# Optimization experiments

Measured on AMD Instinct MI355X. Metric: run time of the kernel, lower is better.

Reference implementation:

```python
import jax, jax.numpy as jnp
import numpy as np

B, S, D = 2, 2048, 1024   # batch, seq, d_model
E, K, H = 8, 4, 1024      # experts, top-k, expert hidden
SH = 2 * H                # shared-expert hidden (n_shared_experts=2)


def setup_inputs() -> dict:
    key = jax.random.key(0)
    ks = jax.random.split(key, 24)
    f = lambda k, shape: jax.random.normal(k, shape, dtype=jnp.float32) * 0.02
    return {
        "x": jax.random.normal(ks[0], (B, S, D), dtype=jnp.float32),
        # Linear(in_features, out_features), stored as [in, out]
        "lin0_w": f(ks[1], (D, D)), "lin0_b": f(ks[2], (D,)),
        "swi1_w1": f(ks[3], (D, D)), "swi1_b1": f(ks[4], (D,)),
        "swi1_w2": f(ks[5], (D, D)), "swi1_b2": f(ks[6], (D,)),
        # MoE router (no bias) + routed experts (SwiGLU FFN, no bias)
        "gate_w": f(ks[7], (E, D)),
        "exp_w1": f(ks[8], (E, D, H)),
        "exp_w3": f(ks[9], (E, D, H)),
        "exp_w2": f(ks[10], (E, H, D)),
        # shared experts fused into one wider SwiGLU MLP (2 shared experts)
        "sh_w1": f(ks[11], (D, SH)),
        "sh_w3": f(ks[12], (D, SH)),
        "sh_w2": f(ks[13], (SH, D)),
        # second Linear + SwiGLU block (num_ff=2)
        "lin1_w": f(ks[14], (D, D)), "lin1_b": f(ks[15], (D,)),
        "swi2_w1": f(ks[16], (D, D)), "swi2_b1": f(ks[17], (D,)),
        "swi2_w2": f(ks[18], (D, D)), "swi2_b2": f(ks[19], (D,)),
    }


def _silu(x):
    return x * jax.nn.sigmoid(x)


def _swiglu(x, w1, b1, w2, b2):
    return _silu(x @ w1 + b1) * (x @ w2 + b2)


def _moe(x, gate_w, exp_w1, exp_w3, exp_w2, sh_w1, sh_w3, sh_w2):
    b, s, d = x.shape
    t = b * s
    xt = x.reshape(t, d)
    # router: softmax scores, greedy top-k, normalized weights (scaling factor = 1)
    scores = jax.nn.softmax(xt @ gate_w.T, axis=-1)          # [T, E]
    topv, topi = jax.lax.top_k(scores, K)                    # [T, K]
    topv = topv / jnp.sum(topv, axis=-1, keepdims=True)
    combine = jnp.zeros((t, E), xt.dtype).at[jnp.arange(t)[:, None], topi].set(topv)  # [T, E]
    # routed experts: SwiGLU FFN per expert, dense-masked combine (same math as dispatch)
    g = _silu(jnp.einsum('td,edh->eth', xt, exp_w1))
    u = jnp.einsum('td,edh->eth', xt, exp_w3)
    yexp = jnp.einsum('eth,ehd->etd', g * u, exp_w2)         # [E, T, D]
    routed = jnp.einsum('te,etd->td', combine, yexp)         # [T, D]
    # shared experts (always on)
    shared = (_silu(xt @ sh_w1) * (xt @ sh_w3)) @ sh_w2      # [T, D]
    return (routed + shared).reshape(b, s, d)


def reference(x, lin0_w, lin0_b, swi1_w1, swi1_b1, swi1_w2, swi1_b2,
              gate_w, exp_w1, exp_w3, exp_w2, sh_w1, sh_w3, sh_w2,
              lin1_w, lin1_b, swi2_w1, swi2_b1, swi2_w2, swi2_b2):
    h = x @ lin0_w + lin0_b
    h = _swiglu(h, swi1_w1, swi1_b1, swi1_w2, swi1_b2)
    h = _moe(h, gate_w, exp_w1, exp_w3, exp_w2, sh_w1, sh_w3, sh_w2)
    h = h @ lin1_w + lin1_b
    h = _swiglu(h, swi2_w1, swi2_b1, swi2_w2, swi2_b2)
    return h
```

## Files before the change

kernel.cpp:

```cpp
#include <hip/hip_runtime.h>
#include <cstdint>
#include <cstddef>

#define T_TOKENS 4096
#define D_MODEL  1024
#define N_EXP    8
#define TOP_K    4
#define H_EXP    1024
#define SH_HID   2048
#define TK       (T_TOKENS*TOP_K)

typedef __bf16 bf16x8 __attribute__((ext_vector_type(8)));
typedef __bf16 bf16x4 __attribute__((ext_vector_type(4)));
typedef float  f32x4  __attribute__((ext_vector_type(4)));

__device__ __forceinline__ float silu_f(float x) {
    return x / (1.0f + expf(-x));
}

template<int NT, bool SEG, bool GATHER, bool GLU>
__global__ __launch_bounds__(256)
void gemm_sp(const float* __restrict__ A, int lda,
             const float* __restrict__ W1, const float* __restrict__ W3,
             int64_t w_estride, int ldw,
             const float* __restrict__ bias1, const float* __restrict__ bias2,
             float* __restrict__ C, __bf16* __restrict__ Cb1, int ldc,
             int M, int Kd,
             const int* __restrict__ seg_off,
             const int* __restrict__ gather)
{
    constexpr int BM = 128, BN = 128, BK = 32;
    __shared__ __bf16 Asl[NT][BM * BK];
    __shared__ __bf16 Bsl[NT][BN * BK];

    int m0, m1, e = 0;
    if (SEG) {
        e = blockIdx.z;
        int s0 = seg_off[e], s1 = seg_off[e + 1];
        m0 = s0 + blockIdx.y * BM;
        if (m0 >= s1) return;
        m1 = (m0 + BM < s1) ? (m0 + BM) : s1;
    } else {
        m0 = blockIdx.y * BM;
        m1 = (m0 + BM < M) ? (m0 + BM) : M;
    }
    const int n0 = blockIdx.x * BN;

    const int tid  = threadIdx.x;
    const int lane = tid & 63;
    const int w    = tid >> 6;
    const int wm   = w >> 1, wn = w & 1;
    const int fr   = lane & 15, fq = lane >> 4;

    const float* aP[4]; int aR[4], aQ[4];
#pragma unroll
    for (int i = 0; i < 4; ++i) {
        int Li = tid + 256 * i;
        int r = Li >> 3, q = Li & 7;
        aR[i] = r; aQ[i] = q;
        int grow = m0 + r;
        if (grow > m1 - 1) grow = m1 - 1;
        if (GATHER) grow = gather[grow];
        aP[i] = A + (int64_t)grow * lda + q * 4;
    }

    const int bn  = tid & 127;
    const int bkh = tid >> 7;
    const float* Wsrc; int wcol;
    if (GLU) {
        int cl = n0 + bn;
        int B  = cl >> 4;
        Wsrc = (B & 1) ? W3 : W1;
        wcol = ((B >> 1) << 4) | (cl & 15);
    } else {
        Wsrc = W1; wcol = n0 + bn;
    }
    const float* Wb = Wsrc + (int64_t)e * w_estride + (int64_t)(bkh * 16) * ldw + wcol;

    f32x4 zero4 = {0.f, 0.f, 0.f, 0.f};
    f32x4 acc[4][4];
#pragma unroll
    for (int i = 0; i < 4; ++i)
#pragma unroll
        for (int j = 0; j < 4; ++j) acc[i][j] = zero4;

    float4 av[4];
    float  wv[16];

#define GLOADS(K0)                                                         \
    do {                                                                   \
        _Pragma("unroll")                                                  \
        for (int i = 0; i < 4; ++i)                                        \
            av[i] = *reinterpret_cast<const float4*>(aP[i] + (K0));        \
        _Pragma("unroll")                                                  \
        for (int j = 0; j < 16; ++j)                                       \
            wv[j] = Wb[(int64_t)((K0) + j) * ldw];                         \
    } while (0)

    const int nk = Kd / BK;
    GLOADS(0);

    for (int ks = 0; ks < nk; ++ks) {
        bf16x4 pa[NT][4];
        bf16x4 pw[NT][4];
#pragma unroll
        for (int i = 0; i < 4; ++i) {
            float vv[4] = {av[i].x, av[i].y, av[i].z, av[i].w};
#pragma unroll
            for (int t = 0; t < 4; ++t) {
                float v = vv[t];
                __bf16 h = (__bf16)v;
                pa[0][i][t] = h;
                if (NT >= 2) {
                    float r = v - (float)h;
                    if (NT == 2) {
                        pa[1][i][t] = (__bf16)r;
                    } else {
                        __bf16 m = (__bf16)r;
                        pa[1][i][t] = m;
                        pa[2][i][t] = (__bf16)(r - (float)m);
                    }
                }
            }
        }
#pragma unroll
        for (int qd = 0; qd < 4; ++qd) {
#pragma unroll
            for (int t = 0; t < 4; ++t) {
                float v = wv[qd * 4 + t];
                __bf16 h = (__bf16)v;
                pw[0][qd][t] = h;
                if (NT >= 2) {
                    float r = v - (float)h;
                    if (NT == 2) {
                        pw[1][qd][t] = (__bf16)r;
                    } else {
                        __bf16 m = (__bf16)r;
                        pw[1][qd][t] = m;
                        pw[2][qd][t] = (__bf16)(r - (float)m);
                    }
                }
            }
        }

        __syncthreads();
#pragma unroll
        for (int i = 0; i < 4; ++i) {
            int r = aR[i], q = aQ[i];
            int c = (q >> 1) ^ ((r >> 1) & 3);
            int idx = r * BK + c * 8 + (q & 1) * 4;
#pragma unroll
            for (int p = 0; p < NT; ++p)
                *reinterpret_cast<bf16x4*>(&Asl[p][idx]) = pa[p][i];
        }
#pragma unroll
        for (int qd = 0; qd < 4; ++qd) {
            int q32 = bkh * 4 + qd;
            int c = (q32 >> 1) ^ ((bn >> 1) & 3);
            int idx = bn * BK + c * 8 + (q32 & 1) * 4;
#pragma unroll
            for (int p = 0; p < NT; ++p)
                *reinterpret_cast<bf16x4*>(&Bsl[p][idx]) = pw[p][qd];
        }

        if (ks + 1 < nk) GLOADS((ks + 1) * BK);
        __syncthreads();

        bf16x8 bfr[NT][4];
#pragma unroll
        for (int p = 0; p < NT; ++p)
#pragma unroll
            for (int j = 0; j < 4; ++j) {
                int rown = wn * 64 + j * 16 + fr;
                int c = fq ^ ((rown >> 1) & 3);
                bfr[p][j] = *reinterpret_cast<const bf16x8*>(&Bsl[p][rown * BK + c * 8]);
            }
#pragma unroll
        for (int im = 0; im < 4; ++im) {
            bf16x8 af[NT];
            int rowm = wm * 64 + im * 16 + fr;
            int c = fq ^ ((rowm >> 1) & 3);
#pragma unroll
            for (int p = 0; p < NT; ++p)
                af[p] = *reinterpret_cast<const bf16x8*>(&Asl[p][rowm * BK + c * 8]);
#pragma unroll
            for (int jn = 0; jn < 4; ++jn) {
                f32x4 a = acc[im][jn];
                a = __builtin_amdgcn_mfma_f32_16x16x32_bf16(af[0], bfr[0][jn], a, 0, 0, 0);
                if (NT >= 2) {
                    a = __builtin_amdgcn_mfma_f32_16x16x32_bf16(af[0], bfr[1][jn], a, 0, 0, 0);
                    a = __builtin_amdgcn_mfma_f32_16x16x32_bf16(af[1], bfr[0][jn], a, 0, 0, 0);
                }
                if (NT == 3) {
                    a = __builtin_amdgcn_mfma_f32_16x16x32_bf16(af[1], bfr[1][jn], a, 0, 0, 0);
                    a = __builtin_amdgcn_mfma_f32_16x16x32_bf16(af[0], bfr[2][jn], a, 0, 0, 0);
                    a = __builtin_amdgcn_mfma_f32_16x16x32_bf16(af[2], bfr[0][jn], a, 0, 0, 0);
                }
                acc[im][jn] = a;
            }
        }
    }
#undef GLOADS

    if (GLU) {
#pragma unroll
        for (int jn = 0; jn < 4; jn += 2) {
            int gcol = (n0 >> 1) + wn * 32 + (jn >> 1) * 16 + fr;
            float bv1 = bias1 ? bias1[gcol] : 0.f;
            float bv2 = bias2 ? bias2[gcol] : 0.f;
#pragma unroll
            for (int im = 0; im < 4; ++im) {
                f32x4 v1 = acc[im][jn];
                f32x4 v2 = acc[im][jn + 1];
#pragma unroll
                for (int r = 0; r < 4; ++r) {
                    int grow = m0 + wm * 64 + im * 16 + fq * 4 + r;
                    if (grow < m1) {
                        float val = silu_f(v1[r] + bv1) * (v2[r] + bv2);
                        int64_t o = (int64_t)grow * ldc + gcol;
                        C[o] = val;
                        if (Cb1) Cb1[o] = (__bf16)val;
                    }
                }
            }
        }
    } else {
#pragma unroll
        for (int jn = 0; jn < 4; ++jn) {
            int col = n0 + wn * 64 + jn * 16 + fr;
            float bv = bias1 ? bias1[col] : 0.f;
#pragma unroll
            for (int im = 0; im < 4; ++im) {
                f32x4 v = acc[im][jn];
#pragma unroll
                for (int r = 0; r < 4; ++r) {
                    int grow = m0 + wm * 64 + im * 16 + fq * 4 + r;
                    if (grow < m1)
                        C[(int64_t)grow * ldc + col] = v[r] + bv;
                }
            }
        }
    }
}

template<bool WBF, bool SEG, bool GATHER, bool GLU, bool EMITB>
__global__ __launch_bounds__(256)
void gemm_bb(const __bf16* __restrict__ A, int lda,
             const void* __restrict__ W1v, const void* __restrict__ W3v,
             int64_t w_estride, int ldw,
             float* __restrict__ C, __bf16* __restrict__ Cb, int ldc,
             int M, int Kd,
             const int* __restrict__ seg_off,
             const int* __restrict__ gather)
{
    constexpr int BM = 128, BN = 128, BK = 32;
    __shared__ __bf16 Asl[BM * BK];
    __shared__ __bf16 Bsl[BN * BK];

    int m0, m1, e = 0;
    if (SEG) {
        e = blockIdx.z;
        int s0 = seg_off[e], s1 = seg_off[e + 1];
        m0 = s0 + blockIdx.y * BM;
        if (m0 >= s1) return;
        m1 = (m0 + BM < s1) ? (m0 + BM) : s1;
    } else {
        m0 = blockIdx.y * BM;
        m1 = (m0 + BM < M) ? (m0 + BM) : M;
    }
    const int n0 = blockIdx.x * BN;

    const int tid  = threadIdx.x;
    const int lane = tid & 63;
    const int w    = tid >> 6;
    const int wm   = w >> 1, wn = w & 1;
    const int fr   = lane & 15, fq = lane >> 4;

    int aWr[2]; const __bf16* Ab[2];
#pragma unroll
    for (int i = 0; i < 2; ++i) {
        int L = tid + 256 * i;
        int r = L >> 2, ch = L & 3;
        aWr[i] = r * BK + (ch ^ ((r >> 1) & 3)) * 8;
        int grow = m0 + r;
        if (grow > m1 - 1) grow = m1 - 1;
        if (GATHER) grow = gather[grow];
        Ab[i] = A + (int64_t)grow * lda + ch * 8;
    }

    const int bn  = tid & 127;
    const int bkh = tid >> 7;
    int wcol; const void* Wsel;
    if (GLU) {
        int cl = n0 + bn;
        int B  = cl >> 4;
        Wsel = (B & 1) ? W3v : W1v;
        wcol = ((B >> 1) << 4) | (cl & 15);
    } else {
        Wsel = W1v; wcol = n0 + bn;
    }
    const __bf16* Wbb = nullptr; const float* Wbf = nullptr;
    if (WBF) Wbb = (const __bf16*)Wsel + (int64_t)e * w_estride + (int64_t)(bkh * 16) * ldw + wcol;
    else     Wbf = (const float*)Wsel + (int64_t)e * w_estride + (int64_t)(bkh * 16) * ldw + wcol;
    int wWr[2];
#pragma unroll
    for (int c = 0; c < 2; ++c)
        wWr[c] = bn * BK + ((bkh * 2 + c) ^ ((bn >> 1) & 3)) * 8;

    f32x4 zero4 = {0.f, 0.f, 0.f, 0.f};
    f32x4 acc[4][4];
#pragma unroll
    for (int i = 0; i < 4; ++i)
#pragma unroll
        for (int j = 0; j < 4; ++j) acc[i][j] = zero4;

    bf16x8 areg[2];
    bf16x8 wreg[2];

#define GLOADS(K0)                                                          \
    do {                                                                    \
        areg[0] = *reinterpret_cast<const bf16x8*>(Ab[0] + (K0));           \
        areg[1] = *reinterpret_cast<const bf16x8*>(Ab[1] + (K0));           \
        if (WBF) {                                                          \
            _Pragma("unroll")                                               \
            for (int j = 0; j < 16; ++j)                                    \
                wreg[j >> 3][j & 7] = Wbb[(int64_t)((K0) + j) * ldw];       \
        } else {                                                            \
            _Pragma("unroll")                                               \
            for (int j = 0; j < 16; ++j)                                    \
                wreg[j >> 3][j & 7] = (__bf16)Wbf[(int64_t)((K0) + j) * ldw]; \
        }                                                                   \
    } while (0)

    const int nk = Kd / BK;
    GLOADS(0);

    for (int ks = 0; ks < nk; ++ks) {
        __syncthreads();
        *reinterpret_cast<bf16x8*>(&Asl[aWr[0]]) = areg[0];
        *reinterpret_cast<bf16x8*>(&Asl[aWr[1]]) = areg[1];
        *reinterpret_cast<bf16x8*>(&Bsl[wWr[0]]) = wreg[0];
        *reinterpret_cast<bf16x8*>(&Bsl[wWr[1]]) = wreg[1];
        if (ks + 1 < nk) GLOADS((ks + 1) * BK);
        __syncthreads();

        bf16x8 bfr[4];
#pragma unroll
        for (int j = 0; j < 4; ++j) {
            int rown = wn * 64 + j * 16 + fr;
            int c = fq ^ ((rown >> 1) & 3);
            bfr[j] = *reinterpret_cast<const bf16x8*>(&Bsl[rown * BK + c * 8]);
        }
#pragma unroll
        for (int im = 0; im < 4; ++im) {
            int rowm = wm * 64 + im * 16 + fr;
            int c = fq ^ ((rowm >> 1) & 3);
            bf16x8 af = *reinterpret_cast<const bf16x8*>(&Asl[rowm * BK + c * 8]);
#pragma unroll
            for (int jn = 0; jn < 4; ++jn)
                acc[im][jn] = __builtin_amdgcn_mfma_f32_16x16x32_bf16(af, bfr[jn], acc[im][jn], 0, 0, 0);
        }
    }
#undef GLOADS

    if (GLU) {
#pragma unroll
        for (int jn = 0; jn < 4; jn += 2) {
            int gcol = (n0 >> 1) + wn * 32 + (jn >> 1) * 16 + fr;
#pragma unroll
            for (int im = 0; im < 4; ++im) {
                f32x4 v1 = acc[im][jn];
                f32x4 v2 = acc[im][jn + 1];
#pragma unroll
                for (int r = 0; r < 4; ++r) {
                    int grow = m0 + wm * 64 + im * 16 + fq * 4 + r;
                    if (grow < m1) {
                        float val = silu_f(v1[r]) * v2[r];
                        int64_t o = (int64_t)grow * ldc + gcol;
                        if (EMITB) Cb[o] = (__bf16)val;
                        else       C[o]  = val;
                    }
                }
            }
        }
    } else {
#pragma unroll
        for (int jn = 0; jn < 4; ++jn) {
            int col = n0 + wn * 64 + jn * 16 + fr;
#pragma unroll
            for (int im = 0; im < 4; ++im) {
                f32x4 v = acc[im][jn];
#pragma unroll
                for (int r = 0; r < 4; ++r) {
                    int grow = m0 + wm * 64 + im * 16 + fq * 4 + r;
                    if (grow < m1)
                        C[(int64_t)grow * ldc + col] = v[r];
                }
            }
        }
    }
}

__global__ void f2b(const float* __restrict__ s, __bf16* __restrict__ d, int64_t n4)
{
    int64_t i = (int64_t)blockIdx.x * blockDim.x + threadIdx.x;
    int64_t st = (int64_t)gridDim.x * blockDim.x;
    for (; i < n4; i += st) {
        float4 v = reinterpret_cast<const float4*>(s)[i];
        bf16x4 o;
        o[0] = (__bf16)v.x; o[1] = (__bf16)v.y;
        o[2] = (__bf16)v.z; o[3] = (__bf16)v.w;
        reinterpret_cast<bf16x4*>(d)[i] = o;
    }
}

__global__ __launch_bounds__(256)
void router_logits(const float* __restrict__ h1, const float* __restrict__ gw,
                   int* __restrict__ topi, float* __restrict__ topw,
                   unsigned char* __restrict__ emask)
{
    const int wave = threadIdx.x >> 6, lane = threadIdx.x & 63;
    const int t = blockIdx.x * 4 + wave;
    const float* x = h1 + (int64_t)t * D_MODEL;
    float part[N_EXP];
#pragma unroll
    for (int e = 0; e < N_EXP; ++e) part[e] = 0.f;
#pragma unroll 4
    for (int i = 0; i < D_MODEL / 64; ++i) {
        int d = lane + 64 * i;
        float xv = x[d];
#pragma unroll
        for (int e = 0; e < N_EXP; ++e)
            part[e] = fmaf(xv, gw[e * D_MODEL + d], part[e]);
    }
#pragma unroll
    for (int m = 32; m > 0; m >>= 1)
#pragma unroll
        for (int e = 0; e < N_EXP; ++e)
            part[e] += __shfl_xor(part[e], m, 64);

    if (lane == 0) {
        float p[N_EXP];
        float mx = -1e30f;
#pragma unroll
        for (int e = 0; e < N_EXP; ++e) mx = part[e] > mx ? part[e] : mx;
        float z = 0.f;
#pragma unroll
        for (int e = 0; e < N_EXP; ++e) { p[e] = expf(part[e] - mx); z += p[e]; }
#pragma unroll
        for (int e = 0; e < N_EXP; ++e) p[e] /= z;
        bool used[N_EXP];
#pragma unroll
        for (int e = 0; e < N_EXP; ++e) used[e] = false;
        int sel[TOP_K]; float sv[TOP_K]; float wsum = 0.f;
        unsigned m8 = 0;
        for (int k = 0; k < TOP_K; ++k) {
            int best = 0; float bvv = -1.f;
            for (int e = 0; e < N_EXP; ++e)
                if (!used[e] && p[e] > bvv) { bvv = p[e]; best = e; }
            used[best] = true; sel[k] = best; sv[k] = bvv; wsum += bvv;
            m8 |= 1u << best;
        }
        for (int k = 0; k < TOP_K; ++k) {
            int idx = t * TOP_K + k;
            topi[idx] = sel[k];
            topw[idx] = sv[k] / wsum;
        }
        emask[t] = (unsigned char)m8;
    }
}

__global__ __launch_bounds__(256)
void rank_local(const unsigned char* __restrict__ emask,
                const int* __restrict__ topi,
                int* __restrict__ pose, int* __restrict__ bh)
{
    const int b = blockIdx.x;
    const int t = b * 256 + threadIdx.x;
    const int wave = threadIdx.x >> 6, lane = threadIdx.x & 63;
    const unsigned m8 = emask[t];

    __shared__ int wcnt[4][N_EXP];
    __shared__ int wbase[4][N_EXP];
    int lrank[N_EXP];
#pragma unroll
    for (int e = 0; e < N_EXP; ++e) {
        unsigned long long bal = __ballot((m8 >> e) & 1u);
        lrank[e] = __popcll(bal & ((1ull << lane) - 1ull));
        if (lane == 0) wcnt[wave][e] = __popcll(bal);
    }
    __syncthreads();
    if (threadIdx.x < N_EXP) {
        int e = threadIdx.x; int a = 0;
        for (int wv = 0; wv < 4; ++wv) { wbase[wv][e] = a; a += wcnt[wv][e]; }
        bh[b * N_EXP + e] = a;
    }
    __syncthreads();
#pragma unroll
    for (int k = 0; k < TOP_K; ++k) {
        int e = topi[t * TOP_K + k];
        pose[t * TOP_K + k] = wbase[wave][e] + lrank[e];
    }
}

__global__ void scan16(const int* __restrict__ bh, int* __restrict__ bb,
                       int* __restrict__ off)
{
    __shared__ int tot[N_EXP];
    if (threadIdx.x < N_EXP) {
        int e = threadIdx.x; int a = 0;
        for (int b = 0; b < 16; ++b) { bb[b * N_EXP + e] = a; a += bh[b * N_EXP + e]; }
        tot[e] = a;
    }
    __syncthreads();
    if (threadIdx.x == 0) {
        int a = 0; off[0] = 0;
        for (int e = 0; e < N_EXP; ++e) { a += tot[e]; off[e + 1] = a; }
    }
}

__global__ __launch_bounds__(256)
void rank_final(const int* __restrict__ topi, const int* __restrict__ pose,
                const int* __restrict__ bb, const int* __restrict__ off,
                int* __restrict__ perm, int* __restrict__ slot_of)
{
    const int b = blockIdx.x;
    const int t = b * 256 + threadIdx.x;
#pragma unroll
    for (int k = 0; k < TOP_K; ++k) {
        int e = topi[t * TOP_K + k];
        int slot = off[e] + bb[b * N_EXP + e] + pose[t * TOP_K + k];
        perm[slot] = t;
        slot_of[t * TOP_K + k] = slot;
    }
}

__global__ __launch_bounds__(256)
void combine_k(const float* __restrict__ y, const float* __restrict__ topw,
               const int* __restrict__ slot_of, float* __restrict__ h2)
{
    int t = blockIdx.x;
    int64_t s[TOP_K]; float w[TOP_K];
#pragma unroll
    for (int k = 0; k < TOP_K; ++k) {
        s[k] = slot_of[t * TOP_K + k];
        w[k] = topw[t * TOP_K + k];
    }
    float* hp = h2 + (int64_t)t * D_MODEL;
    for (int d = threadIdx.x; d < D_MODEL; d += 256) {
        float v = hp[d];
#pragma unroll
        for (int k = 0; k < TOP_K; ++k)
            v = fmaf(w[k], y[s[k] * D_MODEL + d], v);
        hp[d] = v;
    }
}

extern "C" void kernel_launch(void* const* d_in, const int* in_sizes, int n_in,
                              void* d_out, int out_size, void* d_ws, size_t ws_size,
                              hipStream_t stream)
{
    const float* x      = (const float*)d_in[0];
    const float* lin0_w = (const float*)d_in[1];
    const float* lin0_b = (const float*)d_in[2];
    const float* s1w1   = (const float*)d_in[3];
    const float* s1b1   = (const float*)d_in[4];
    const float* s1w2   = (const float*)d_in[5];
    const float* s1b2   = (const float*)d_in[6];
    const float* gate_w = (const float*)d_in[7];
    const float* ew1    = (const float*)d_in[8];
    const float* ew3    = (const float*)d_in[9];
    const float* ew2    = (const float*)d_in[10];
    const float* shw1   = (const float*)d_in[11];
    const float* shw3   = (const float*)d_in[12];
    const float* shw2   = (const float*)d_in[13];
    const float* lin1_w = (const float*)d_in[14];
    const float* lin1_b = (const float*)d_in[15];
    const float* s2w1   = (const float*)d_in[16];
    const float* s2b1   = (const float*)d_in[17];
    const float* s2w2   = (const float*)d_in[18];
    const float* s2b2   = (const float*)d_in[19];
    float* out = (float*)d_out;

    char* ws = (char*)d_ws;
    const size_t MB = 1024 * 1024;
    dim3 blk(256);
    const int64_t ES = (int64_t)D_MODEL * H_EXP;
    const bool full = ws_size >= (size_t)216 * MB;

    float* h0   = (float*)(ws + 0 * MB);
    float* h1   = (float*)(ws + 16 * MB);
    float* h2   = (float*)(ws + 32 * MB);
    float* yexp = (float*)(ws + 48 * MB);
    __bf16* gu_b  = (__bf16*)(ws + 112 * MB);
    __bf16* gsh_b = (__bf16*)(ws + 112 * MB);
    __bf16* h1b   = (__bf16*)(ws + 144 * MB);
    __bf16* ewt1 = (__bf16*)(ws + 152 * MB);
    __bf16* ewt3 = (__bf16*)(ws + 168 * MB);
    __bf16* ewt2 = (__bf16*)(ws + 184 * MB);
    __bf16* shb1 = (__bf16*)(ws + 200 * MB);
    __bf16* shb3 = (__bf16*)(ws + 204 * MB);
    __bf16* shb2 = (__bf16*)(ws + 208 * MB);
    char* sm = ws + (full ? 212 * MB : 152 * MB);
    int*   topi    = (int*)(sm);
    float* topw    = (float*)(sm + 64 * 1024);
    int*   pose    = (int*)(sm + 128 * 1024);
    int*   slot_of = (int*)(sm + 192 * 1024);
    int*   perm    = (int*)(sm + 256 * 1024);
    int*   bh      = (int*)(sm + 320 * 1024);
    int*   bb      = (int*)(sm + 321 * 1024);
    int*   off     = (int*)(sm + 322 * 1024);
    unsigned char* emask = (unsigned char*)(sm + 323 * 1024);

    gemm_sp<3, false, false, false><<<dim3(8, 32, 1), blk, 0, stream>>>(
        x, D_MODEL, lin0_w, nullptr, 0, D_MODEL, lin0_b, nullptr,
        h0, nullptr, D_MODEL, T_TOKENS, D_MODEL, nullptr, nullptr);

    gemm_sp<3, false, false, true><<<dim3(16, 32, 1), blk, 0, stream>>>(
        h0, D_MODEL, s1w1, s1w2, 0, D_MODEL, s1b1, s1b2,
        h1, h1b, D_MODEL, T_TOKENS, D_MODEL, nullptr, nullptr);

    router_logits<<<T_TOKENS / 4, blk, 0, stream>>>(h1, gate_w, topi, topw, emask);
    rank_local<<<16, blk, 0, stream>>>(emask, topi, pose, bh);
    scan16<<<1, 64, 0, stream>>>(bh, bb, off);
    rank_final<<<16, blk, 0, stream>>>(topi, pose, bb, off, perm, slot_of);

    if (full) {
        f2b<<<1024, blk, 0, stream>>>(ew1,  ewt1, (int64_t)N_EXP * ES / 4);
        f2b<<<1024, blk, 0, stream>>>(ew3,  ewt3, (int64_t)N_EXP * ES / 4);
        f2b<<<1024, blk, 0, stream>>>(ew2,  ewt2, (int64_t)N_EXP * ES / 4);
        f2b<<<1024, blk, 0, stream>>>(shw1, shb1, (int64_t)D_MODEL * SH_HID / 4);
        f2b<<<1024, blk, 0, stream>>>(shw3, shb3, (int64_t)D_MODEL * SH_HID / 4);
        f2b<<<1024, blk, 0, stream>>>(shw2, shb2, (int64_t)SH_HID * D_MODEL / 4);

        gemm_bb<true, true, true, true, true><<<dim3(16, 128, N_EXP), blk, 0, stream>>>(
            h1b, D_MODEL, ewt1, ewt3, ES, H_EXP,
            nullptr, gu_b, H_EXP, 0, D_MODEL, off, perm);
        gemm_bb<true, true, false, false, false><<<dim3(8, 128, N_EXP), blk, 0, stream>>>(
            gu_b, H_EXP, ewt2, nullptr, (int64_t)H_EXP * D_MODEL, D_MODEL,
            yexp, nullptr, D_MODEL, 0, H_EXP, off, nullptr);
        gemm_bb<true, false, false, true, true><<<dim3(32, 32, 1), blk, 0, stream>>>(
            h1b, D_MODEL, shb1, shb3, 0, SH_HID,
            nullptr, gsh_b, SH_HID, T_TOKENS, D_MODEL, nullptr, nullptr);
        gemm_bb<true, false, false, false, false><<<dim3(8, 32, 1), blk, 0, stream>>>(
            gsh_b, SH_HID, shb2, nullptr, 0, D_MODEL,
            h2, nullptr, D_MODEL, T_TOKENS, SH_HID, nullptr, nullptr);
    } else {
        gemm_bb<false, true, true, true, true><<<dim3(16, 128, N_EXP), blk, 0, stream>>>(
            h1b, D_MODEL, ew1, ew3, ES, H_EXP,
            nullptr, gu_b, H_EXP, 0, D_MODEL, off, perm);
        gemm_bb<false, true, false, false, false><<<dim3(8, 128, N_EXP), blk, 0, stream>>>(
            gu_b, H_EXP, ew2, nullptr, (int64_t)H_EXP * D_MODEL, D_MODEL,
            yexp, nullptr, D_MODEL, 0, H_EXP, off, nullptr);
        gemm_bb<false, false, false, true, true><<<dim3(32, 32, 1), blk, 0, stream>>>(
            h1b, D_MODEL, shw1, shw3, 0, SH_HID,
            nullptr, gsh_b, SH_HID, T_TOKENS, D_MODEL, nullptr, nullptr);
        gemm_bb<false, false, false, false, false><<<dim3(8, 32, 1), blk, 0, stream>>>(
            gsh_b, SH_HID, shw2, nullptr, 0, D_MODEL,
            h2, nullptr, D_MODEL, T_TOKENS, SH_HID, nullptr, nullptr);
    }

    combine_k<<<T_TOKENS, blk, 0, stream>>>(yexp, topw, slot_of, h2);

    gemm_sp<2, false, false, false><<<dim3(8, 32, 1), blk, 0, stream>>>(
        h2, D_MODEL, lin1_w, nullptr, 0, D_MODEL, lin1_b, nullptr,
        h0, nullptr, D_MODEL, T_TOKENS, D_MODEL, nullptr, nullptr);

    gemm_sp<2, false, false, true><<<dim3(16, 32, 1), blk, 0, stream>>>(
        h0, D_MODEL, s2w1, s2w2, 0, D_MODEL, s2b1, s2b2,
        out, nullptr, D_MODEL, T_TOKENS, D_MODEL, nullptr, nullptr);
}
```

Baseline: 679.7 us.

## Transpose bf16 weights for vectorized loads; move post-MoE GEMMs to bf16 path

The fp32-to-bf16 weight conversion now also transposes each weight to [out,in], so the bf16 GEMM loads each weight chunk as one 16-byte vector instead of 16 strided scalar loads. Expert outputs are stored in bf16, and the combine kernel is vectorized and emits a bf16 activation. The last Linear and SwiGLU are moved from the split-precision GEMM to the bf16 MFMA GEMM, which gains bias support in its epilogue. The transposes add extra conversion work per call, and the lower-precision intermediates may change numerical accuracy.

```diff
diff --git a/kernel.cpp b/kernel.cpp
--- a/kernel.cpp
+++ b/kernel.cpp
@@ -248,6 +248,7 @@
 void gemm_bb(const __bf16* __restrict__ A, int lda,
              const void* __restrict__ W1v, const void* __restrict__ W3v,
              int64_t w_estride, int ldw,
+             const float* __restrict__ bias1, const float* __restrict__ bias2,
              float* __restrict__ C, __bf16* __restrict__ Cb, int ldc,
              int M, int Kd,
              const int* __restrict__ seg_off,
@@ -288,24 +289,45 @@
         Ab[i] = A + (int64_t)grow * lda + ch * 8;
     }
 
-    const int bn  = tid & 127;
-    const int bkh = tid >> 7;
-    int wcol; const void* Wsel;
-    if (GLU) {
-        int cl = n0 + bn;
-        int B  = cl >> 4;
-        Wsel = (B & 1) ? W3v : W1v;
-        wcol = ((B >> 1) << 4) | (cl & 15);
+    int wR[2]; const __bf16* Wt[2];
+    const float* Wbf = nullptr;
+    int wWrS[2];
+    if (WBF) {
+#pragma unroll
+        for (int i = 0; i < 2; ++i) {
+            int L = tid + 256 * i;
+            int nl = L >> 2, ch = L & 3;
+            wR[i] = nl * BK + (ch ^ ((nl >> 1) & 3)) * 8;
+            int cl = n0 + nl;
+            const __bf16* base;
+            int srcrow;
+            if (GLU) {
+                int B = cl >> 4;
+                base = (const __bf16*)((B & 1) ? W3v : W1v);
+                srcrow = ((B >> 1) << 4) | (cl & 15);
+            } else {
+                base = (const __bf16*)W1v;
+                srcrow = cl;
+            }
+            Wt[i] = base + (int64_t)e * w_estride + (int64_t)srcrow * ldw + ch * 8;
+        }
     } else {
-        Wsel = W1v; wcol = n0 + bn;
-    }
-    const __bf16* Wbb = nullptr; const float* Wbf = nullptr;
-    if (WBF) Wbb = (const __bf16*)Wsel + (int64_t)e * w_estride + (int64_t)(bkh * 16) * ldw + wcol;
-    else     Wbf = (const float*)Wsel + (int64_t)e * w_estride + (int64_t)(bkh * 16) * ldw + wcol;
-    int wWr[2];
-#pragma unroll
-    for (int c = 0; c < 2; ++c)
-        wWr[c] = bn * BK + ((bkh * 2 + c) ^ ((bn >> 1) & 3)) * 8;
+        const int bn  = tid & 127;
+        const int bkh = tid >> 7;
+        int wcol; const void* Wsel;
+        if (GLU) {
+            int cl = n0 + bn;
+            int B  = cl >> 4;
+            Wsel = (B & 1) ? W3v : W1v;
+            wcol = ((B >> 1) << 4) | (cl & 15);
+        } else {
+            Wsel = W1v; wcol = n0 + bn;
+        }
+        Wbf = (const float*)Wsel + (int64_t)e * w_estride + (int64_t)(bkh * 16) * ldw + wcol;
+#pragma unroll
+        for (int c = 0; c < 2; ++c)
+            wWrS[c] = bn * BK + ((bkh * 2 + c) ^ ((bn >> 1) & 3)) * 8;
+    }
 
     f32x4 zero4 = {0.f, 0.f, 0.f, 0.f};
     f32x4 acc[4][4];
@@ -322,9 +344,8 @@
         areg[0] = *reinterpret_cast<const bf16x8*>(Ab[0] + (K0));           \
         areg[1] = *reinterpret_cast<const bf16x8*>(Ab[1] + (K0));           \
         if (WBF) {                                                          \
-            _Pragma("unroll")                                               \
-            for (int j = 0; j < 16; ++j)                                    \
-                wreg[j >> 3][j & 7] = Wbb[(int64_t)((K0) + j) * ldw];       \
+            wreg[0] = *reinterpret_cast<const bf16x8*>(Wt[0] + (K0));       \
+            wreg[1] = *reinterpret_cast<const bf16x8*>(Wt[1] + (K0));       \
         } else {                                                            \
             _Pragma("unroll")                                               \
             for (int j = 0; j < 16; ++j)                                    \
@@ -339,8 +360,13 @@
         __syncthreads();
         *reinterpret_cast<bf16x8*>(&Asl[aWr[0]]) = areg[0];
         *reinterpret_cast<bf16x8*>(&Asl[aWr[1]]) = areg[1];
-        *reinterpret_cast<bf16x8*>(&Bsl[wWr[0]]) = wreg[0];
-        *reinterpret_cast<bf16x8*>(&Bsl[wWr[1]]) = wreg[1];
+        if (WBF) {
+            *reinterpret_cast<bf16x8*>(&Bsl[wR[0]]) = wreg[0];
+            *reinterpret_cast<bf16x8*>(&Bsl[wR[1]]) = wreg[1];
+        } else {
+            *reinterpret_cast<bf16x8*>(&Bsl[wWrS[0]]) = wreg[0];
+            *reinterpret_cast<bf16x8*>(&Bsl[wWrS[1]]) = wreg[1];
+        }
         if (ks + 1 < nk) GLOADS((ks + 1) * BK);
         __syncthreads();
 
@@ -367,6 +393,8 @@
 #pragma unroll
         for (int jn = 0; jn < 4; jn += 2) {
             int gcol = (n0 >> 1) + wn * 32 + (jn >> 1) * 16 + fr;
+            float bv1 = bias1 ? bias1[gcol] : 0.f;
+            float bv2 = bias2 ? bias2[gcol] : 0.f;
 #pragma unroll
             for (int im = 0; im < 4; ++im) {
                 f32x4 v1 = acc[im][jn];
@@ -375,7 +403,7 @@
                 for (int r = 0; r < 4; ++r) {
                     int grow = m0 + wm * 64 + im * 16 + fq * 4 + r;
                     if (grow < m1) {
-                        float val = silu_f(v1[r]) * v2[r];
+                        float val = silu_f(v1[r] + bv1) * (v2[r] + bv2);
                         int64_t o = (int64_t)grow * ldc + gcol;
                         if (EMITB) Cb[o] = (__bf16)val;
                         else       C[o]  = val;
@@ -387,30 +415,42 @@
 #pragma unroll
         for (int jn = 0; jn < 4; ++jn) {
             int col = n0 + wn * 64 + jn * 16 + fr;
+            float bv = bias1 ? bias1[col] : 0.f;
 #pragma unroll
             for (int im = 0; im < 4; ++im) {
                 f32x4 v = acc[im][jn];
 #pragma unroll
                 for (int r = 0; r < 4; ++r) {
                     int grow = m0 + wm * 64 + im * 16 + fq * 4 + r;
-                    if (grow < m1)
-                        C[(int64_t)grow * ldc + col] = v[r];
+                    if (grow < m1) {
+                        int64_t o = (int64_t)grow * ldc + col;
+                        if (EMITB) Cb[o] = (__bf16)(v[r] + bv);
+                        else       C[o]  = v[r] + bv;
+                    }
                 }
             }
         }
     }
 }
 
-__global__ void f2b(const float* __restrict__ s, __bf16* __restrict__ d, int64_t n4)
-{
-    int64_t i = (int64_t)blockIdx.x * blockDim.x + threadIdx.x;
-    int64_t st = (int64_t)gridDim.x * blockDim.x;
-    for (; i < n4; i += st) {
-        float4 v = reinterpret_cast<const float4*>(s)[i];
-        bf16x4 o;
-        o[0] = (__bf16)v.x; o[1] = (__bf16)v.y;
-        o[2] = (__bf16)v.z; o[3] = (__bf16)v.w;
-        reinterpret_cast<bf16x4*>(d)[i] = o;
+__global__ __launch_bounds__(256)
+void f2bT(const float* __restrict__ src, __bf16* __restrict__ dst, int R, int C)
+{
+    __shared__ float t[32][33];
+    const int64_t eoff = (int64_t)blockIdx.z * R * C;
+    src += eoff; dst += eoff;
+    const int c0 = blockIdx.x * 32, r0 = blockIdx.y * 32;
+    const int tx = threadIdx.x & 31, ty = threadIdx.x >> 5;
+#pragma unroll
+    for (int i = 0; i < 4; ++i) {
+        int r = r0 + ty + i * 8;
+        t[ty + i * 8][tx] = src[(int64_t)r * C + c0 + tx];
+    }
+    __syncthreads();
+#pragma unroll
+    for (int i = 0; i < 4; ++i) {
+        int c = c0 + ty + i * 8;
+        dst[(int64_t)c * R + r0 + tx] = (__bf16)t[tx][ty + i * 8];
     }
 }
 
@@ -535,24 +575,46 @@
     }
 }
 
+template<bool YB>
 __global__ __launch_bounds__(256)
-void combine_k(const float* __restrict__ y, const float* __restrict__ topw,
-               const int* __restrict__ slot_of, float* __restrict__ h2)
+void combine_k(const void* __restrict__ yv, const float* __restrict__ topw,
+               const int* __restrict__ slot_of, float* __restrict__ h2,
+               __bf16* __restrict__ h2b)
 {
     int t = blockIdx.x;
-    int64_t s[TOP_K]; float w[TOP_K];
+    int64_t s[TOP_K]; float wgt[TOP_K];
 #pragma unroll
     for (int k = 0; k < TOP_K; ++k) {
         s[k] = slot_of[t * TOP_K + k];
-        w[k] = topw[t * TOP_K + k];
-    }
-    float* hp = h2 + (int64_t)t * D_MODEL;
-    for (int d = threadIdx.x; d < D_MODEL; d += 256) {
-        float v = hp[d];
-#pragma unroll
-        for (int k = 0; k < TOP_K; ++k)
-            v = fmaf(w[k], y[s[k] * D_MODEL + d], v);
-        hp[d] = v;
+        wgt[k] = topw[t * TOP_K + k];
+    }
+    int64_t base4 = ((int64_t)t * D_MODEL) / 4 + threadIdx.x;
+    float4 v = reinterpret_cast<const float4*>(h2)[base4];
+#pragma unroll
+    for (int k = 0; k < TOP_K; ++k) {
+        float yy[4];
+        if (YB) {
+            bf16x4 yb = reinterpret_cast<const bf16x4*>((const __bf16*)yv)
+                            [s[k] * (D_MODEL / 4) + threadIdx.x];
+            yy[0] = (float)yb[0]; yy[1] = (float)yb[1];
+            yy[2] = (float)yb[2]; yy[3] = (float)yb[3];
+        } else {
+            float4 yf = reinterpret_cast<const float4*>((const float*)yv)
+                            [s[k] * (D_MODEL / 4) + threadIdx.x];
+            yy[0] = yf.x; yy[1] = yf.y; yy[2] = yf.z; yy[3] = yf.w;
+        }
+        v.x = fmaf(wgt[k], yy[0], v.x);
+        v.y = fmaf(wgt[k], yy[1], v.y);
+        v.z = fmaf(wgt[k], yy[2], v.z);
+        v.w = fmaf(wgt[k], yy[3], v.w);
+    }
+    if (h2b) {
+        bf16x4 o;
+        o[0] = (__bf16)v.x; o[1] = (__bf16)v.y;
+        o[2] = (__bf16)v.z; o[3] = (__bf16)v.w;
+        reinterpret_cast<bf16x4*>(h2b)[base4] = o;
+    } else {
+        reinterpret_cast<float4*>(h2)[base4] = v;
     }
 }
 
@@ -588,85 +650,130 @@
     const int64_t ES = (int64_t)D_MODEL * H_EXP;
     const bool full = ws_size >= (size_t)216 * MB;
 
-    float* h0   = (float*)(ws + 0 * MB);
-    float* h1   = (float*)(ws + 16 * MB);
-    float* h2   = (float*)(ws + 32 * MB);
-    float* yexp = (float*)(ws + 48 * MB);
-    __bf16* gu_b  = (__bf16*)(ws + 112 * MB);
-    __bf16* gsh_b = (__bf16*)(ws + 112 * MB);
-    __bf16* h1b   = (__bf16*)(ws + 144 * MB);
-    __bf16* ewt1 = (__bf16*)(ws + 152 * MB);
-    __bf16* ewt3 = (__bf16*)(ws + 168 * MB);
-    __bf16* ewt2 = (__bf16*)(ws + 184 * MB);
-    __bf16* shb1 = (__bf16*)(ws + 200 * MB);
-    __bf16* shb3 = (__bf16*)(ws + 204 * MB);
-    __bf16* shb2 = (__bf16*)(ws + 208 * MB);
-    char* sm = ws + (full ? 212 * MB : 152 * MB);
-    int*   topi    = (int*)(sm);
-    float* topw    = (float*)(sm + 64 * 1024);
-    int*   pose    = (int*)(sm + 128 * 1024);
-    int*   slot_of = (int*)(sm + 192 * 1024);
-    int*   perm    = (int*)(sm + 256 * 1024);
-    int*   bh      = (int*)(sm + 320 * 1024);
-    int*   bb      = (int*)(sm + 321 * 1024);
-    int*   off     = (int*)(sm + 322 * 1024);
-    unsigned char* emask = (unsigned char*)(sm + 323 * 1024);
-
-    gemm_sp<3, false, false, false><<<dim3(8, 32, 1), blk, 0, stream>>>(
-        x, D_MODEL, lin0_w, nullptr, 0, D_MODEL, lin0_b, nullptr,
-        h0, nullptr, D_MODEL, T_TOKENS, D_MODEL, nullptr, nullptr);
-
-    gemm_sp<3, false, false, true><<<dim3(16, 32, 1), blk, 0, stream>>>(
-        h0, D_MODEL, s1w1, s1w2, 0, D_MODEL, s1b1, s1b2,
-        h1, h1b, D_MODEL, T_TOKENS, D_MODEL, nullptr, nullptr);
-
-    router_logits<<<T_TOKENS / 4, blk, 0, stream>>>(h1, gate_w, topi, topw, emask);
-    rank_local<<<16, blk, 0, stream>>>(emask, topi, pose, bh);
-    scan16<<<1, 64, 0, stream>>>(bh, bb, off);
-    rank_final<<<16, blk, 0, stream>>>(topi, pose, bb, off, perm, slot_of);
+    float* h0 = (float*)(ws + 0 * MB);
+    float* h1 = (float*)(ws + 16 * MB);
+    float* h2 = (float*)(ws + 32 * MB);
 
     if (full) {
-        f2b<<<1024, blk, 0, stream>>>(ew1,  ewt1, (int64_t)N_EXP * ES / 4);
-        f2b<<<1024, blk, 0, stream>>>(ew3,  ewt3, (int64_t)N_EXP * ES / 4);
-        f2b<<<1024, blk, 0, stream>>>(ew2,  ewt2, (int64_t)N_EXP * ES / 4);
-        f2b<<<1024, blk, 0, stream>>>(shw1, shb1, (int64_t)D_MODEL * SH_HID / 4);
-        f2b<<<1024, blk, 0, stream>>>(shw3, shb3, (int64_t)D_MODEL * SH_HID / 4);
-        f2b<<<1024, blk, 0, stream>>>(shw2, shb2, (int64_t)SH_HID * D_MODEL / 4);
+        __bf16* yexp_b = (__bf16*)(ws + 48 * MB);
+        __bf16* gu_b   = (__bf16*)(ws + 80 * MB);
+        __bf16* gsh_b  = gu_b;
+        __bf16* h1b    = (__bf16*)(ws + 112 * MB);
+        __bf16* h2b    = (__bf16*)(ws + 120 * MB);
+        __bf16* h3b    = (__bf16*)(ws + 128 * MB);
+        __bf16* e1T = (__bf16*)(ws + 136 * MB);
+        __bf16* e3T = (__bf16*)(ws + 152 * MB);
+        __bf16* e2T = (__bf16*)(ws + 168 * MB);
+        __bf16* s1T = (__bf16*)(ws + 184 * MB);
+        __bf16* s3T = (__bf16*)(ws + 188 * MB);
+        __bf16* s2T = (__bf16*)(ws + 192 * MB);
+        __bf16* l1T = (__bf16*)(ws + 196 * MB);
+        __bf16* q1T = (__bf16*)(ws + 198 * MB);
+        __bf16* q2T = (__bf16*)(ws + 200 * MB);
+        char* sm = ws + 202 * MB;
+        int*   topi    = (int*)(sm);
+        float* topw    = (float*)(sm + 64 * 1024);
+        int*   pose    = (int*)(sm + 128 * 1024);
+        int*   slot_of = (int*)(sm + 192 * 1024);
+        int*   perm    = (int*)(sm + 256 * 1024);
+        int*   bh      = (int*)(sm + 320 * 1024);
+        int*   bb      = (int*)(sm + 321 * 1024);
+        int*   off     = (int*)(sm + 322 * 1024);
+        unsigned char* emask = (unsigned char*)(sm + 323 * 1024);
+
+        f2bT<<<dim3(32, 32, N_EXP), blk, 0, stream>>>(ew1, e1T, D_MODEL, H_EXP);
+        f2bT<<<dim3(32, 32, N_EXP), blk, 0, stream>>>(ew3, e3T, D_MODEL, H_EXP);
+        f2bT<<<dim3(32, 32, N_EXP), blk, 0, stream>>>(ew2, e2T, H_EXP, D_MODEL);
+        f2bT<<<dim3(64, 32, 1), blk, 0, stream>>>(shw1, s1T, D_MODEL, SH_HID);
+        f2bT<<<dim3(64, 32, 1), blk, 0, stream>>>(shw3, s3T, D_MODEL, SH_HID);
+        f2bT<<<dim3(32, 64, 1), blk, 0, stream>>>(shw2, s2T, SH_HID, D_MODEL);
+        f2bT<<<dim3(32, 32, 1), blk, 0, stream>>>(lin1_w, l1T, D_MODEL, D_MODEL);
+        f2bT<<<dim3(32, 32, 1), blk, 0, stream>>>(s2w1, q1T, D_MODEL, D_MODEL);
+        f2bT<<<dim3(32, 32, 1), blk, 0, stream>>>(s2w2, q2T, D_MODEL, D_MODEL);
+
+        gemm_sp<3, false, false, false><<<dim3(8, 32, 1), blk, 0, stream>>>(
+            x, D_MODEL, lin0_w, nullptr, 0, D_MODEL, lin0_b, nullptr,
+            h0, nullptr, D_MODEL, T_TOKENS, D_MODEL, nullptr, nullptr);
+
+        gemm_sp<3, false, false, true><<<dim3(16, 32, 1), blk, 0, stream>>>(
+            h0, D_MODEL, s1w1, s1w2, 0, D_MODEL, s1b1, s1b2,
+            h1, h1b, D_MODEL, T_TOKENS, D_MODEL, nullptr, nullptr);
+
+        router_logits<<<T_TOKENS / 4, blk, 0, stream>>>(h1, gate_w, topi, topw, emask);
+        rank_local<<<16, blk, 0, stream>>>(emask, topi, pose, bh);
+        scan16<<<1, 64, 0, stream>>>(bh, bb, off);
+        rank_final<<<16, blk, 0, stream>>>(topi, pose, bb, off, perm, slot_of);
 
         gemm_bb<true, true, true, true, true><<<dim3(16, 128, N_EXP), blk, 0, stream>>>(
-            h1b, D_MODEL, ewt1, ewt3, ES, H_EXP,
+            h1b, D_MODEL, e1T, e3T, ES, D_MODEL, nullptr, nullptr,
             nullptr, gu_b, H_EXP, 0, D_MODEL, off, perm);
-        gemm_bb<true, true, false, false, false><<<dim3(8, 128, N_EXP), blk, 0, stream>>>(
-            gu_b, H_EXP, ewt2, nullptr, (int64_t)H_EXP * D_MODEL, D_MODEL,
-            yexp, nullptr, D_MODEL, 0, H_EXP, off, nullptr);
+        gemm_bb<true, true, false, false, true><<<dim3(8, 128, N_EXP), blk, 0, stream>>>(
+            gu_b, H_EXP, e2T, nullptr, ES, H_EXP, nullptr, nullptr,
+            nullptr, yexp_b, D_MODEL, 0, H_EXP, off, nullptr);
         gemm_bb<true, false, false, true, true><<<dim3(32, 32, 1), blk, 0, stream>>>(
-            h1b, D_MODEL, shb1, shb3, 0, SH_HID,
+            h1b, D_MODEL, s1T, s3T, 0, D_MODEL, nullptr, nullptr,
             nullptr, gsh_b, SH_HID, T_TOKENS, D_MODEL, nullptr, nullptr);
         gemm_bb<true, false, false, false, false><<<dim3(8, 32, 1), blk, 0, stream>>>(
-            gsh_b, SH_HID, shb2, nullptr, 0, D_MODEL,
+            gsh_b, SH_HID, s2T, nullptr, 0, SH_HID, nullptr, nullptr,
             h2, nullptr, D_MODEL, T_TOKENS, SH_HID, nullptr, nullptr);
+
+        combine_k<true><<<T_TOKENS, blk, 0, stream>>>(yexp_b, topw, slot_of, h2, h2b);
+
+        gemm_bb<true, false, false, false, true><<<dim3(8, 32, 1), blk, 0, stream>>>(
+            h2b, D_MODEL, l1T, nullptr, 0, D_MODEL, lin1_b, nullptr,
+            nullptr, h3b, D_MODEL, T_TOKENS, D_MODEL, nullptr, nullptr);
+
+        gemm_bb<true, false, false, true, false><<<dim3(16, 32, 1), blk, 0, stream>>>(
+            h3b, D_MODEL, q1T, q2T, 0, D_MODEL, s2b1, s2b2,
+            out, nullptr, D_MODEL, T_TOKENS, D_MODEL, nullptr, nullptr);
     } else {
+        float* yexp  = (float*)(ws + 48 * MB);
+        __bf16* gu_b = (__bf16*)(ws + 112 * MB);
+        __bf16* gsh_b = gu_b;
+        __bf16* h1b  = (__bf16*)(ws + 144 * MB);
+        char* sm = ws + 152 * MB;
+        int*   topi    = (int*)(sm);
+        float* topw    = (float*)(sm + 64 * 1024);
+        int*   pose    = (int*)(sm + 128 * 1024);
+        int*   slot_of = (int*)(sm + 192 * 1024);
+        int*   perm    = (int*)(sm + 256 * 1024);
+        int*   bh      = (int*)(sm + 320 * 1024);
+        int*   bb      = (int*)(sm + 321 * 1024);
+        int*   off     = (int*)(sm + 322 * 1024);
+        unsigned char* emask = (unsigned char*)(sm + 323 * 1024);
+
+        gemm_sp<3, false, false, false><<<dim3(8, 32, 1), blk, 0, stream>>>(
+            x, D_MODEL, lin0_w, nullptr, 0, D_MODEL, lin0_b, nullptr,
+            h0, nullptr, D_MODEL, T_TOKENS, D_MODEL, nullptr, nullptr);
+        gemm_sp<3, false, false, true><<<dim3(16, 32, 1), blk, 0, stream>>>(
+            h0, D_MODEL, s1w1, s1w2, 0, D_MODEL, s1b1, s1b2,
+            h1, h1b, D_MODEL, T_TOKENS, D_MODEL, nullptr, nullptr);
+
+        router_logits<<<T_TOKENS / 4, blk, 0, stream>>>(h1, gate_w, topi, topw, emask);
+        rank_local<<<16, blk, 0, stream>>>(emask, topi, pose, bh);
+        scan16<<<1, 64, 0, stream>>>(bh, bb, off);
+        rank_final<<<16, blk, 0, stream>>>(topi, pose, bb, off, perm, slot_of);
+
         gemm_bb<false, true, true, true, true><<<dim3(16, 128, N_EXP), blk, 0, stream>>>(
-            h1b, D_MODEL, ew1, ew3, ES, H_EXP,
+            h1b, D_MODEL, ew1, ew3, ES, H_EXP, nullptr, nullptr,
             nullptr, gu_b, H_EXP, 0, D_MODEL, off, perm);
         gemm_bb<false, true, false, false, false><<<dim3(8, 128, N_EXP), blk, 0, stream>>>(
-            gu_b, H_EXP, ew2, nullptr, (int64_t)H_EXP * D_MODEL, D_MODEL,
+            gu_b, H_EXP, ew2, nullptr, (int64_t)H_EXP * D_MODEL, D_MODEL, nullptr, nullptr,
             yexp, nullptr, D_MODEL, 0, H_EXP, off, nullptr);
         gemm_bb<false, false, false, true, true><<<dim3(32, 32, 1), blk, 0, stream>>>(
-            h1b, D_MODEL, shw1, shw3, 0, SH_HID,
+            h1b, D_MODEL, shw1, shw3, 0, SH_HID, nullptr, nullptr,
             nullptr, gsh_b, SH_HID, T_TOKENS, D_MODEL, nullptr, nullptr);
         gemm_bb<false, false, false, false, false><<<dim3(8, 32, 1), blk, 0, stream>>>(
-            gsh_b, SH_HID, shw2, nullptr, 0, D_MODEL,
+            gsh_b, SH_HID, shw2, nullptr, 0, D_MODEL, nullptr, nullptr,
             h2, nullptr, D_MODEL, T_TOKENS, SH_HID, nullptr, nullptr);
-    }
-
-    combine_k<<<T_TOKENS, blk, 0, stream>>>(yexp, topw, slot_of, h2);
-
-    gemm_sp<2, false, false, false><<<dim3(8, 32, 1), blk, 0, stream>>>(
-        h2, D_MODEL, lin1_w, nullptr, 0, D_MODEL, lin1_b, nullptr,
-        h0, nullptr, D_MODEL, T_TOKENS, D_MODEL, nullptr, nullptr);
-
-    gemm_sp<2, false, false, true><<<dim3(16, 32, 1), blk, 0, stream>>>(
-        h0, D_MODEL, s2w1, s2w2, 0, D_MODEL, s2b1, s2b2,
-        out, nullptr, D_MODEL, T_TOKENS, D_MODEL, nullptr, nullptr);
-}
+
+        combine_k<false><<<T_TOKENS, blk, 0, stream>>>(yexp, topw, slot_of, h2, nullptr);
+
+        gemm_sp<2, false, false, false><<<dim3(8, 32, 1), blk, 0, stream>>>(
+            h2, D_MODEL, lin1_w, nullptr, 0, D_MODEL, lin1_b, nullptr,
+            h0, nullptr, D_MODEL, T_TOKENS, D_MODEL, nullptr, nullptr);
+        gemm_sp<2, false, false, true><<<dim3(16, 32, 1), blk, 0, stream>>>(
+            h0, D_MODEL, s2w1, s2w2, 0, D_MODEL, s2b1, s2b2,
+            out, nullptr, D_MODEL, T_TOKENS, D_MODEL, nullptr, nullptr);
+    }
+}
```

Measured after the change: 600.5 us. 1.13x faster.
